# Kernel optimization log

Measured on AMD Instinct MI355X. Metric: run time of the kernel, lower is better.

## Reference

```python
import jax, jax.numpy as jnp
import numpy as np

# irreps_in = irreps_out = 32x0e + 16x1o ; irreps_sh = 1x0e + 1x1o
MUL0, MUL1 = 32, 16
N_NODES = 12000
N_EDGES = 120000
INV_SQRT3 = float(1.0 / np.sqrt(3.0))   # w3j(1,1,0), w3j(0,1,1), w3j(1,0,1) coefficient
SQRT2 = float(np.sqrt(2.0))             # e3nn normalize2mom constant for ReLU
# e3nn TP norms: irrep_normalization='component', path_normalization='element'.
# Each output irrep receives paths with num_elements 32 and 16 -> x = 48.
N_0E = float(1.0 / np.sqrt(48.0))       # alpha = dim(0e)/48 = 1/48
N_1O = float(np.sqrt(3.0 / 48.0))       # alpha = dim(1o)/48 = 3/48
# uvw weight blocks (mul2 = 1): (s,y0->s),(s,y0->g),(v,y1->s),(v,y1->g),(s,y1->v),(v,y0->v)
SPLITS = [MUL0 * MUL0, MUL0 * MUL1, MUL1 * MUL0, MUL1 * MUL1, MUL0 * MUL1, MUL1 * MUL1]
OFFS = np.cumsum([0] + SPLITS)
WNUM = int(OFFS[-1])  # 3072


def setup_inputs() -> dict:
    key = jax.random.key(0)
    k1, k2, k3, k4, k5 = jax.random.split(key, 5)
    x = jax.random.normal(k1, (N_NODES, MUL0 + 3 * MUL1), dtype=jnp.float32)
    edge_attr = jax.random.normal(k2, (N_EDGES, 64), dtype=jnp.float32)
    Yij = jax.random.normal(k3, (N_EDGES, 4), dtype=jnp.float32)
    edge_index = jax.random.randint(k4, (2, N_EDGES), 0, N_NODES, dtype=jnp.int64)
    w_emb = jax.random.normal(k5, (2 * MUL0 + 64, WNUM), dtype=jnp.float32)
    return {"x": x, "edge_attr": edge_attr, "Yij": Yij,
            "edge_index": edge_index, "w_emb": w_emb}


def reference(x, edge_attr, Yij, edge_index, w_emb):
    dst, src = edge_index[0], edge_index[1]
    E = edge_attr.shape[0]
    xs = x[:, :MUL0]                                   # [N, 32] scalars (0e)
    xv = x[:, MUL0:].reshape(-1, MUL1, 3)              # [N, 16, 3] vectors (1o)

    # per-edge weight MLP (single e3nn FC layer, weight scaled by 1/sqrt(fan_in))
    emb = jnp.concatenate([xs[dst], xs[src], edge_attr], axis=-1)     # [E, 128]
    w = emb @ (w_emb / np.sqrt(w_emb.shape[0]))                       # [E, 3072]
    Ws = [w[:, OFFS[i]:OFFS[i + 1]] for i in range(6)]
    W1 = Ws[0].reshape(E, MUL0, MUL0)
    W2 = Ws[1].reshape(E, MUL0, MUL1)
    W3 = Ws[2].reshape(E, MUL1, MUL0)
    W4 = Ws[3].reshape(E, MUL1, MUL1)
    W5 = Ws[4].reshape(E, MUL0, MUL1)
    W6 = Ws[5].reshape(E, MUL1, MUL1)

    # gather source features, split sh
    x1s, x1v = xs[src], xv[src]                        # [E,32], [E,16,3]
    y0, y1 = Yij[:, 0], Yij[:, 1:4]                    # [E], [E,3]

    sy0 = x1s * y0[:, None]                            # 0e x 0e paths
    vdot = jnp.einsum('euk,ek->eu', x1v, y1) * INV_SQRT3  # 1o x 1o -> 0e
    out_s = N_0E * (jnp.einsum('euw,eu->ew', W1, sy0) +
                    jnp.einsum('euw,eu->ew', W3, vdot))    # [E, 32]
    out_g = N_0E * (jnp.einsum('euw,eu->ew', W2, sy0) +
                    jnp.einsum('euw,eu->ew', W4, vdot))    # [E, 16]
    out_v = (N_1O * INV_SQRT3) * (
        jnp.einsum('euw,eu,ek->ewk', W5, x1s, y1) +
        jnp.einsum('euw,euk->ewk', W6, x1v * y0[:, None, None]))  # [E, 16, 3]

    msg = jnp.concatenate([out_s, out_g, out_v.reshape(E, MUL1 * 3)], axis=-1)  # [E, 96]

    # scatter mean onto destination nodes
    summed = jax.ops.segment_sum(msg, dst, num_segments=N_NODES)
    cnt = jax.ops.segment_sum(jnp.ones((E,), msg.dtype), dst, num_segments=N_NODES)
    mean = summed / jnp.maximum(cnt, 1.0)[:, None]

    # Gate (e3nn Activation normalizes ReLU by sqrt(2))
    s = SQRT2 * jax.nn.relu(mean[:, :MUL0])
    g = SQRT2 * jax.nn.relu(mean[:, MUL0:MUL0 + MUL1])
    v = mean[:, MUL0 + MUL1:].reshape(-1, MUL1, 3) * g[:, :, None]
    out = jnp.concatenate([s, v.reshape(-1, MUL1 * 3)], axis=-1)     # [N, 80]
    return x + out
```

## Files before the change

kernel.cpp:

```cpp
#include <hip/hip_runtime.h>
#include <hip/hip_bf16.h>

#define E_EDGES 120000
#define NUM_NODES 12000

typedef __attribute__((ext_vector_type(8))) short bfrag;
typedef __attribute__((ext_vector_type(8))) unsigned short ushort8;
typedef __attribute__((ext_vector_type(4))) float f32x4;

#define INV_SQRT3 0.57735026918962576f
#define SQRT2_C   1.41421356237309515f
#define N_0E_C    0.14433756729740643f
#define NV_C      0.14433756729740643f
#define WSCALE    0.08838834764831845f

__device__ __forceinline__ unsigned short f2bf(float f) {
    union { float f; unsigned int u; } v; v.f = f;
    unsigned int r = v.u + 0x7fffu + ((v.u >> 16) & 1u);
    return (unsigned short)(r >> 16);
}

__device__ __forceinline__ ushort8 pack8(f32x4 a, f32x4 b) {
    ushort8 o;
    o[0] = f2bf(a.x); o[1] = f2bf(a.y); o[2] = f2bf(a.z); o[3] = f2bf(a.w);
    o[4] = f2bf(b.x); o[5] = f2bf(b.y); o[6] = f2bf(b.z); o[7] = f2bf(b.w);
    return o;
}

__global__ void k_wt(const float* __restrict__ w_emb, unsigned short* __restrict__ Bt) {
    int o = blockIdx.x * 256 + threadIdx.x;
    if (o >= 3072 * 128) return;
    int t = o >> 11;
    int c = (o >> 3) & 255;
    int j = o & 7;
    int kb = c >> 6;
    int quad = (c >> 4) & 3;
    int col = c & 15;
    int k = kb * 32 + quad * 8 + j;
    int n = t * 16 + col;
    Bt[o] = f2bf(w_emb[k * 3072 + n] * WSCALE);
}

__global__ void k_prep(const float* __restrict__ x, const float* __restrict__ edge_attr,
                       const float* __restrict__ Yij, const int* __restrict__ edge_index,
                       unsigned short* __restrict__ emb, float* __restrict__ rT,
                       float* __restrict__ cnt) {
    int e = blockIdx.x * 256 + threadIdx.x;
    if (e >= E_EDGES) return;
    int dst = edge_index[e];
    int src = edge_index[E_EDGES + e];
    f32x4 y = *(const f32x4*)(Yij + 4 * (long)e);
    float y0 = y.x, y1a = y.y, y1b = y.z, y1c = y.w;
    const float* xd = x + (long)dst * 80;
    const float* xs = x + (long)src * 80;
    const float* ea = edge_attr + (long)e * 64;

    ushort8* embp = (ushort8*)(emb + (long)e * 128);

    float xsv[80];
#pragma unroll
    for (int i = 0; i < 80; i += 4) {
        f32x4 v = *(const f32x4*)(xs + i);
        xsv[i] = v.x; xsv[i + 1] = v.y; xsv[i + 2] = v.z; xsv[i + 3] = v.w;
    }
#pragma unroll
    for (int cb = 0; cb < 4; ++cb) {
        f32x4 a = *(const f32x4*)(xd + cb * 8);
        f32x4 b = *(const f32x4*)(xd + cb * 8 + 4);
        embp[cb] = pack8(a, b);
    }
#pragma unroll
    for (int cb = 0; cb < 4; ++cb) {
        f32x4 a, b;
        a.x = xsv[cb * 8 + 0]; a.y = xsv[cb * 8 + 1]; a.z = xsv[cb * 8 + 2]; a.w = xsv[cb * 8 + 3];
        b.x = xsv[cb * 8 + 4]; b.y = xsv[cb * 8 + 5]; b.z = xsv[cb * 8 + 6]; b.w = xsv[cb * 8 + 7];
        embp[4 + cb] = pack8(a, b);
    }
#pragma unroll
    for (int cb = 0; cb < 8; ++cb) {
        f32x4 a = *(const f32x4*)(ea + cb * 8);
        f32x4 b = *(const f32x4*)(ea + cb * 8 + 4);
        embp[8 + cb] = pack8(a, b);
    }
#pragma unroll
    for (int u = 0; u < 32; ++u) rT[(long)u * E_EDGES + e] = xsv[u] * y0;
#pragma unroll
    for (int u = 0; u < 16; ++u)
        rT[(long)(32 + u) * E_EDGES + e] =
            (xsv[32 + 3 * u] * y1a + xsv[33 + 3 * u] * y1b + xsv[34 + 3 * u] * y1c) * INV_SQRT3;
#pragma unroll
    for (int u = 0; u < 32; ++u) rT[(long)(48 + u) * E_EDGES + e] = xsv[u];
#pragma unroll
    for (int j = 0; j < 48; ++j) rT[(long)(80 + j) * E_EDGES + e] = xsv[32 + j] * y0;
    atomicAdd(cnt + dst, 1.0f);
}

__global__ __launch_bounds__(256, 4) void k_gemm(
    const unsigned short* __restrict__ emb, const unsigned short* __restrict__ Bt,
    const float* __restrict__ rT, const int* __restrict__ edge_index,
    const float* __restrict__ Yij, float* __restrict__ summed) {
    const int lane = threadIdx.x & 63;
    const int wave = threadIdx.x >> 6;
    const int phase = blockIdx.x & 1;
    long e0 = (long)(blockIdx.x >> 1) * 128 + (long)wave * 32;
    const bool dup = (e0 + 32 > E_EDGES);
    if (dup) e0 = E_EDGES - 32;
    const int col = lane & 15, quad = lane >> 4;

    __shared__ __align__(16) char lds[2][16384];

    bfrag A[2][4];
#pragma unroll
    for (int s = 0; s < 2; ++s) {
        const unsigned short* ap = emb + (e0 + s * 16 + col) * 128 + quad * 8;
#pragma unroll
        for (int kb = 0; kb < 4; ++kb) A[s][kb] = *(const bfrag*)(ap + kb * 32);
    }

    auto stage = [&](int ci) {
        const char* g = (const char*)Bt + (size_t)ci * 16384 + wave * 4096 + lane * 16;
        char* l = &lds[ci & 1][wave * 4096];
#pragma unroll
        for (int j = 0; j < 4; ++j)
            __builtin_amdgcn_global_load_lds(
                (const __attribute__((address_space(1))) unsigned int*)(g + j * 1024),
                (__attribute__((address_space(3))) unsigned int*)(l + j * 1024), 16, 0, 0);
    };

    f32x4 z = {0.f, 0.f, 0.f, 0.f};

    const float* rbase = rT + e0 + quad * 4;
    auto loadw = [&](int r, f32x4& a, f32x4& b) {
        const float* p = rbase + (long)r * E_EDGES;
        a = *(const f32x4*)(p);
        b = *(const f32x4*)(p + 16);
    };

    auto tile = [&](const char* lt, f32x4& c0, f32x4& c1) {
        bfrag B0 = *(const bfrag*)(lt + lane * 16);
        bfrag B1 = *(const bfrag*)(lt + lane * 16 + 1024);
        bfrag B2 = *(const bfrag*)(lt + lane * 16 + 2048);
        bfrag B3 = *(const bfrag*)(lt + lane * 16 + 3072);
        c0 = z; c1 = z;
        c0 = __builtin_amdgcn_mfma_f32_16x16x32_bf16(A[0][0], B0, c0, 0, 0, 0);
        c1 = __builtin_amdgcn_mfma_f32_16x16x32_bf16(A[1][0], B0, c1, 0, 0, 0);
        c0 = __builtin_amdgcn_mfma_f32_16x16x32_bf16(A[0][1], B1, c0, 0, 0, 0);
        c1 = __builtin_amdgcn_mfma_f32_16x16x32_bf16(A[1][1], B1, c1, 0, 0, 0);
        c0 = __builtin_amdgcn_mfma_f32_16x16x32_bf16(A[0][2], B2, c0, 0, 0, 0);
        c1 = __builtin_amdgcn_mfma_f32_16x16x32_bf16(A[1][2], B2, c1, 0, 0, 0);
        c0 = __builtin_amdgcn_mfma_f32_16x16x32_bf16(A[0][3], B3, c0, 0, 0, 0);
        c1 = __builtin_amdgcn_mfma_f32_16x16x32_bf16(A[1][3], B3, c1, 0, 0, 0);
    };

    int bufp = 0;
    auto nextbuf = [&](int nxt) -> const char* {
        __syncthreads();
        if (nxt >= 0) stage(nxt);
        const char* b = lds[bufp & 1];
        ++bufp;
        return b;
    };

    f32x4 c0, c1;

    if (phase == 0) {
        f32x4 acc_s0[2] = {z, z}, acc_s1[2] = {z, z};
        stage(0);
        {
            f32x4 p0a, p0b, p1a, p1b;
            loadw(0, p0a, p0b); loadw(1, p1a, p1b);
#pragma unroll 1
            for (int j = 0; j < 16; ++j) {
                const char* buf = nextbuf(j < 15 ? j + 1 : 24);
                f32x4 w0a = p0a, w0b = p0b, w1a = p1a, w1b = p1b;
                int nr = (j < 15) ? (2 * j + 2) : 32;
                loadw(nr, p0a, p0b); loadw(nr + 1, p1a, p1b);
                tile(buf,         c0, c1); acc_s0[0] += c0 * w0a; acc_s0[1] += c1 * w0b;
                tile(buf + 4096,  c0, c1); acc_s1[0] += c0 * w0a; acc_s1[1] += c1 * w0b;
                tile(buf + 8192,  c0, c1); acc_s0[0] += c0 * w1a; acc_s0[1] += c1 * w1b;
                tile(buf + 12288, c0, c1); acc_s1[0] += c0 * w1a; acc_s1[1] += c1 * w1b;
            }
        }
        {
            f32x4 p0a, p0b, p1a, p1b;
            loadw(32, p0a, p0b); loadw(33, p1a, p1b);
#pragma unroll 1
            for (int j = 0; j < 8; ++j) {
                const char* buf = nextbuf(j < 7 ? 25 + j : -1);
                f32x4 w0a = p0a, w0b = p0b, w1a = p1a, w1b = p1b;
                int nr = (j < 7) ? (32 + 2 * j + 2) : 32;
                loadw(nr, p0a, p0b); loadw(nr + 1, p1a, p1b);
                tile(buf,         c0, c1); acc_s0[0] += c0 * w0a; acc_s0[1] += c1 * w0b;
                tile(buf + 4096,  c0, c1); acc_s1[0] += c0 * w0a; acc_s1[1] += c1 * w0b;
                tile(buf + 8192,  c0, c1); acc_s0[0] += c0 * w1a; acc_s0[1] += c1 * w1b;
                tile(buf + 12288, c0, c1); acc_s1[0] += c0 * w1a; acc_s1[1] += c1 * w1b;
            }
        }
        if (dup) return;
#pragma unroll
        for (int s = 0; s < 2; ++s) {
            long eb = e0 + s * 16 + quad * 4;
#pragma unroll
            for (int r = 0; r < 4; ++r) {
                int d = edge_index[eb + r];
                float* base = summed + (long)d * 96;
                atomicAdd(base + col,      N_0E_C * acc_s0[s][r]);
                atomicAdd(base + col + 16, N_0E_C * acc_s1[s][r]);
            }
        }
    } else {
        f32x4 acc_g[2] = {z, z}, acc_t5[2] = {z, z};
        f32x4 acc_v[2][3] = {{z, z, z}, {z, z, z}};
        stage(16);
        {
            f32x4 pa[4], pb[4];
#pragma unroll
            for (int i = 0; i < 4; ++i) loadw(i, pa[i], pb[i]);
#pragma unroll 1
            for (int j = 0; j < 8; ++j) {
                const char* buf = nextbuf(j < 7 ? 17 + j : 32);
                f32x4 wa[4], wb[4];
#pragma unroll
                for (int i = 0; i < 4; ++i) { wa[i] = pa[i]; wb[i] = pb[i]; }
                int nr = (j < 7) ? (4 * j + 4) : 32;
#pragma unroll
                for (int i = 0; i < 4; ++i) loadw(nr + i, pa[i], pb[i]);
#pragma unroll
                for (int i = 0; i < 4; ++i) {
                    tile(buf + i * 4096, c0, c1);
                    acc_g[0] += c0 * wa[i]; acc_g[1] += c1 * wb[i];
                }
            }
        }
        {
            f32x4 pa[4], pb[4];
#pragma unroll
            for (int i = 0; i < 4; ++i) loadw(32 + i, pa[i], pb[i]);
#pragma unroll 1
            for (int j = 0; j < 4; ++j) {
                const char* buf = nextbuf(33 + j);
                f32x4 wa[4], wb[4];
#pragma unroll
                for (int i = 0; i < 4; ++i) { wa[i] = pa[i]; wb[i] = pb[i]; }
                int nr = (j < 3) ? (32 + 4 * j + 4) : 48;
#pragma unroll
                for (int i = 0; i < 4; ++i) loadw(nr + i, pa[i], pb[i]);
#pragma unroll
                for (int i = 0; i < 4; ++i) {
                    tile(buf + i * 4096, c0, c1);
                    acc_g[0] += c0 * wa[i]; acc_g[1] += c1 * wb[i];
                }
            }
        }
        {
            f32x4 pa[4], pb[4];
#pragma unroll
            for (int i = 0; i < 4; ++i) loadw(48 + i, pa[i], pb[i]);
#pragma unroll 1
            for (int j = 0; j < 8; ++j) {
                const char* buf = nextbuf(37 + j);
                f32x4 wa[4], wb[4];
#pragma unroll
                for (int i = 0; i < 4; ++i) { wa[i] = pa[i]; wb[i] = pb[i]; }
                int nr = (j < 7) ? (48 + 4 * j + 4) : 48;
#pragma unroll
                for (int i = 0; i < 4; ++i) loadw(nr + i, pa[i], pb[i]);
#pragma unroll
                for (int i = 0; i < 4; ++i) {
                    tile(buf + i * 4096, c0, c1);
                    acc_t5[0] += c0 * wa[i]; acc_t5[1] += c1 * wb[i];
                }
            }
        }
        {
            f32x4 va[3], vb[3];
#pragma unroll
            for (int k = 0; k < 3; ++k) loadw(80 + k, va[k], vb[k]);
#pragma unroll 1
            for (int j = 0; j < 4; ++j) {
                const char* buf = nextbuf(j < 3 ? 45 + j : -1);
#pragma unroll
                for (int i = 0; i < 4; ++i) {
                    f32x4 wa[3], wb[3];
#pragma unroll
                    for (int k = 0; k < 3; ++k) { wa[k] = va[k]; wb[k] = vb[k]; }
                    int un = 4 * j + i + 1; if (un > 15) un = 0;
#pragma unroll
                    for (int k = 0; k < 3; ++k) loadw(80 + 3 * un + k, va[k], vb[k]);
                    tile(buf + i * 4096, c0, c1);
#pragma unroll
                    for (int k = 0; k < 3; ++k) {
                        acc_v[0][k] += c0 * wa[k];
                        acc_v[1][k] += c1 * wb[k];
                    }
                }
            }
        }
        if (dup) return;
#pragma unroll
        for (int s = 0; s < 2; ++s) {
            long eb = e0 + s * 16 + quad * 4;
#pragma unroll
            for (int r = 0; r < 4; ++r) {
                long e = eb + r;
                int d = edge_index[e];
                float* base = summed + (long)d * 96;
                float y1a = Yij[4 * e + 1], y1b = Yij[4 * e + 2], y1c = Yij[4 * e + 3];
                atomicAdd(base + 32 + col, N_0E_C * acc_g[s][r]);
                float t5 = acc_t5[s][r];
                atomicAdd(base + 48 + col * 3 + 0, NV_C * (t5 * y1a + acc_v[s][0][r]));
                atomicAdd(base + 48 + col * 3 + 1, NV_C * (t5 * y1b + acc_v[s][1][r]));
                atomicAdd(base + 48 + col * 3 + 2, NV_C * (t5 * y1c + acc_v[s][2][r]));
            }
        }
    }
}

__global__ void k_final(const float* __restrict__ x, const float* __restrict__ summed,
                        const float* __restrict__ cnt, float* __restrict__ out) {
    int tid = blockIdx.x * 256 + threadIdx.x;
    if (tid >= NUM_NODES * 80) return;
    int n = tid / 80, c = tid % 80;
    float m = fmaxf(cnt[n], 1.0f);
    float inv = 1.0f / m;
    float val;
    if (c < 32) {
        val = SQRT2_C * fmaxf(summed[(long)n * 96 + c] * inv, 0.0f);
    } else {
        int j = c - 32;
        int w = j / 3;
        float g = SQRT2_C * fmaxf(summed[(long)n * 96 + 32 + w] * inv, 0.0f);
        val = summed[(long)n * 96 + 48 + j] * inv * g;
    }
    out[tid] = x[tid] + val;
}

extern "C" void kernel_launch(void* const* d_in, const int* in_sizes, int n_in,
                              void* d_out, int out_size, void* d_ws, size_t ws_size,
                              hipStream_t stream) {
    const float* x         = (const float*)d_in[0];
    const float* edge_attr = (const float*)d_in[1];
    const float* Yij       = (const float*)d_in[2];
    const int*   edge_index= (const int*)d_in[3];
    const float* w_emb     = (const float*)d_in[4];
    float* out = (float*)d_out;

    char* ws = (char*)d_ws;
    size_t off = 0;
    unsigned short* emb = (unsigned short*)(ws + off); off += (size_t)E_EDGES * 128 * 2;
    unsigned short* Bt  = (unsigned short*)(ws + off); off += (size_t)3072 * 128 * 2;
    off = (off + 255) & ~(size_t)255;
    float* rT     = (float*)(ws + off); off += (size_t)128 * E_EDGES * 4;
    size_t zoff = off;
    float* summed = (float*)(ws + off); off += (size_t)NUM_NODES * 96 * 4;
    float* cnt    = (float*)(ws + off); off += (size_t)NUM_NODES * 4;

    hipMemsetAsync(ws + zoff, 0, (size_t)NUM_NODES * 97 * 4, stream);
    k_wt  <<<(3072 * 128 + 255) / 256, 256, 0, stream>>>(w_emb, Bt);
    k_prep<<<(E_EDGES + 255) / 256, 256, 0, stream>>>(x, edge_attr, Yij, edge_index, emb, rT, cnt);
    k_gemm<<<2 * ((E_EDGES + 127) / 128), 256, 0, stream>>>(emb, Bt, rT, edge_index, Yij, summed);
    k_final<<<(NUM_NODES * 80 + 255) / 256, 256, 0, stream>>>(x, summed, cnt, out);
}
```

Before: 293.8 us.

## Tile rT per 32-edge block, double LDS stage size, coalesce weight transpose

Stores the per-edge coefficient array rT as contiguous 32-edge by 128-row blocks instead of row-major over all edges, so each wave's coefficient loads hit a compact 16KB region. The GEMM now stages 32KB chunks of the weight matrix into LDS per barrier, which halves the number of __syncthreads, and launch bounds drop to 2 blocks per SM to fit the larger LDS. The weight transpose kernel now reads w_emb coalesced and scatters the writes. Possible costs are lower occupancy and fewer overlapping waves.

```diff
diff --git a/kernel.cpp b/kernel.cpp
--- a/kernel.cpp
+++ b/kernel.cpp
@@ -28,17 +28,13 @@
 }
 
 __global__ void k_wt(const float* __restrict__ w_emb, unsigned short* __restrict__ Bt) {
-    int o = blockIdx.x * 256 + threadIdx.x;
-    if (o >= 3072 * 128) return;
-    int t = o >> 11;
-    int c = (o >> 3) & 255;
-    int j = o & 7;
-    int kb = c >> 6;
-    int quad = (c >> 4) & 3;
-    int col = c & 15;
-    int k = kb * 32 + quad * 8 + j;
-    int n = t * 16 + col;
-    Bt[o] = f2bf(w_emb[k * 3072 + n] * WSCALE);
+    int i = blockIdx.x * 256 + threadIdx.x;
+    if (i >= 128 * 3072) return;
+    int k = i / 3072;
+    int n = i - k * 3072;
+    int t = n >> 4, col = n & 15;
+    int kb = k >> 5, quad = (k >> 3) & 3, j = k & 7;
+    Bt[(size_t)t * 2048 + (size_t)(kb * 64 + quad * 16 + col) * 8 + j] = f2bf(w_emb[i] * WSCALE);
 }
 
 __global__ void k_prep(const float* __restrict__ x, const float* __restrict__ edge_attr,
@@ -56,6 +52,7 @@
     const float* ea = edge_attr + (long)e * 64;
 
     ushort8* embp = (ushort8*)(emb + (long)e * 128);
+    float* rb = rT + (long)(e >> 5) * 4096 + (e & 31);
 
     float xsv[80];
 #pragma unroll
@@ -83,19 +80,19 @@
         embp[8 + cb] = pack8(a, b);
     }
 #pragma unroll
-    for (int u = 0; u < 32; ++u) rT[(long)u * E_EDGES + e] = xsv[u] * y0;
+    for (int u = 0; u < 32; ++u) rb[u * 32] = xsv[u] * y0;
 #pragma unroll
     for (int u = 0; u < 16; ++u)
-        rT[(long)(32 + u) * E_EDGES + e] =
+        rb[(32 + u) * 32] =
             (xsv[32 + 3 * u] * y1a + xsv[33 + 3 * u] * y1b + xsv[34 + 3 * u] * y1c) * INV_SQRT3;
 #pragma unroll
-    for (int u = 0; u < 32; ++u) rT[(long)(48 + u) * E_EDGES + e] = xsv[u];
-#pragma unroll
-    for (int j = 0; j < 48; ++j) rT[(long)(80 + j) * E_EDGES + e] = xsv[32 + j] * y0;
+    for (int u = 0; u < 32; ++u) rb[(48 + u) * 32] = xsv[u];
+#pragma unroll
+    for (int j = 0; j < 48; ++j) rb[(80 + j) * 32] = xsv[32 + j] * y0;
     atomicAdd(cnt + dst, 1.0f);
 }
 
-__global__ __launch_bounds__(256, 4) void k_gemm(
+__global__ __launch_bounds__(256, 2) void k_gemm(
     const unsigned short* __restrict__ emb, const unsigned short* __restrict__ Bt,
     const float* __restrict__ rT, const int* __restrict__ edge_index,
     const float* __restrict__ Yij, float* __restrict__ summed) {
@@ -107,7 +104,7 @@
     if (dup) e0 = E_EDGES - 32;
     const int col = lane & 15, quad = lane >> 4;
 
-    __shared__ __align__(16) char lds[2][16384];
+    __shared__ __align__(16) char lds[2][32768];
 
     bfrag A[2][4];
 #pragma unroll
@@ -117,21 +114,26 @@
         for (int kb = 0; kb < 4; ++kb) A[s][kb] = *(const bfrag*)(ap + kb * 32);
     }
 
+    int wp = 0, rp = 0;
     auto stage = [&](int ci) {
-        const char* g = (const char*)Bt + (size_t)ci * 16384 + wave * 4096 + lane * 16;
-        char* l = &lds[ci & 1][wave * 4096];
-#pragma unroll
-        for (int j = 0; j < 4; ++j)
+        const char* g = (const char*)Bt + (size_t)ci * 32768 + wave * 8192 + lane * 16;
+        char* l = &lds[(wp++) & 1][wave * 8192];
+#pragma unroll
+        for (int j = 0; j < 8; ++j)
             __builtin_amdgcn_global_load_lds(
                 (const __attribute__((address_space(1))) unsigned int*)(g + j * 1024),
                 (__attribute__((address_space(3))) unsigned int*)(l + j * 1024), 16, 0, 0);
     };
+    auto nextbuf = [&](int nxt) -> const char* {
+        __syncthreads();
+        if (nxt >= 0) stage(nxt);
+        return lds[(rp++) & 1];
+    };
 
     f32x4 z = {0.f, 0.f, 0.f, 0.f};
-
-    const float* rbase = rT + e0 + quad * 4;
+    const float* rbase = rT + ((e0 >> 5) * 4096) + quad * 4;
     auto loadw = [&](int r, f32x4& a, f32x4& b) {
-        const float* p = rbase + (long)r * E_EDGES;
+        const float* p = rbase + r * 32;
         a = *(const f32x4*)(p);
         b = *(const f32x4*)(p + 16);
     };
@@ -152,49 +154,51 @@
         c1 = __builtin_amdgcn_mfma_f32_16x16x32_bf16(A[1][3], B3, c1, 0, 0, 0);
     };
 
-    int bufp = 0;
-    auto nextbuf = [&](int nxt) -> const char* {
-        __syncthreads();
-        if (nxt >= 0) stage(nxt);
-        const char* b = lds[bufp & 1];
-        ++bufp;
-        return b;
-    };
-
     f32x4 c0, c1;
 
     if (phase == 0) {
         f32x4 acc_s0[2] = {z, z}, acc_s1[2] = {z, z};
+        f32x4 ca[4], cb[4], na[4], nb[4];
         stage(0);
-        {
-            f32x4 p0a, p0b, p1a, p1b;
-            loadw(0, p0a, p0b); loadw(1, p1a, p1b);
-#pragma unroll 1
-            for (int j = 0; j < 16; ++j) {
-                const char* buf = nextbuf(j < 15 ? j + 1 : 24);
-                f32x4 w0a = p0a, w0b = p0b, w1a = p1a, w1b = p1b;
-                int nr = (j < 15) ? (2 * j + 2) : 32;
-                loadw(nr, p0a, p0b); loadw(nr + 1, p1a, p1b);
-                tile(buf,         c0, c1); acc_s0[0] += c0 * w0a; acc_s0[1] += c1 * w0b;
-                tile(buf + 4096,  c0, c1); acc_s1[0] += c0 * w0a; acc_s1[1] += c1 * w0b;
-                tile(buf + 8192,  c0, c1); acc_s0[0] += c0 * w1a; acc_s0[1] += c1 * w1b;
-                tile(buf + 12288, c0, c1); acc_s1[0] += c0 * w1a; acc_s1[1] += c1 * w1b;
-            }
-        }
-        {
-            f32x4 p0a, p0b, p1a, p1b;
-            loadw(32, p0a, p0b); loadw(33, p1a, p1b);
-#pragma unroll 1
-            for (int j = 0; j < 8; ++j) {
-                const char* buf = nextbuf(j < 7 ? 25 + j : -1);
-                f32x4 w0a = p0a, w0b = p0b, w1a = p1a, w1b = p1b;
-                int nr = (j < 7) ? (32 + 2 * j + 2) : 32;
-                loadw(nr, p0a, p0b); loadw(nr + 1, p1a, p1b);
-                tile(buf,         c0, c1); acc_s0[0] += c0 * w0a; acc_s0[1] += c1 * w0b;
-                tile(buf + 4096,  c0, c1); acc_s1[0] += c0 * w0a; acc_s1[1] += c1 * w0b;
-                tile(buf + 8192,  c0, c1); acc_s0[0] += c0 * w1a; acc_s0[1] += c1 * w1b;
-                tile(buf + 12288, c0, c1); acc_s1[0] += c0 * w1a; acc_s1[1] += c1 * w1b;
-            }
+#pragma unroll
+        for (int i = 0; i < 4; ++i) loadw(i, ca[i], cb[i]);
+#pragma unroll 1
+        for (int bc = 0; bc < 8; ++bc) {
+            const char* buf = nextbuf(bc < 7 ? bc + 1 : 12);
+            int nr = (bc < 7) ? 4 * bc + 4 : 32;
+#pragma unroll
+            for (int i = 0; i < 4; ++i) loadw(nr + i, na[i], nb[i]);
+#pragma unroll
+            for (int h = 0; h < 2; ++h) {
+                const char* hb = buf + h * 16384;
+                f32x4 w0a = ca[2 * h], w0b = cb[2 * h];
+                f32x4 w1a = ca[2 * h + 1], w1b = cb[2 * h + 1];
+                tile(hb,         c0, c1); acc_s0[0] += c0 * w0a; acc_s0[1] += c1 * w0b;
+                tile(hb + 4096,  c0, c1); acc_s1[0] += c0 * w0a; acc_s1[1] += c1 * w0b;
+                tile(hb + 8192,  c0, c1); acc_s0[0] += c0 * w1a; acc_s0[1] += c1 * w1b;
+                tile(hb + 12288, c0, c1); acc_s1[0] += c0 * w1a; acc_s1[1] += c1 * w1b;
+            }
+#pragma unroll
+            for (int i = 0; i < 4; ++i) { ca[i] = na[i]; cb[i] = nb[i]; }
+        }
+#pragma unroll 1
+        for (int bc = 0; bc < 4; ++bc) {
+            const char* buf = nextbuf(bc < 3 ? 13 + bc : -1);
+            int nr = (bc < 3) ? 36 + 4 * bc : 32;
+#pragma unroll
+            for (int i = 0; i < 4; ++i) loadw(nr + i, na[i], nb[i]);
+#pragma unroll
+            for (int h = 0; h < 2; ++h) {
+                const char* hb = buf + h * 16384;
+                f32x4 w0a = ca[2 * h], w0b = cb[2 * h];
+                f32x4 w1a = ca[2 * h + 1], w1b = cb[2 * h + 1];
+                tile(hb,         c0, c1); acc_s0[0] += c0 * w0a; acc_s0[1] += c1 * w0b;
+                tile(hb + 4096,  c0, c1); acc_s1[0] += c0 * w0a; acc_s1[1] += c1 * w0b;
+                tile(hb + 8192,  c0, c1); acc_s0[0] += c0 * w1a; acc_s0[1] += c1 * w1b;
+                tile(hb + 12288, c0, c1); acc_s1[0] += c0 * w1a; acc_s1[1] += c1 * w1b;
+            }
+#pragma unroll
+            for (int i = 0; i < 4; ++i) { ca[i] = na[i]; cb[i] = nb[i]; }
         }
         if (dup) return;
 #pragma unroll
@@ -211,14 +215,16 @@
     } else {
         f32x4 acc_g[2] = {z, z}, acc_t5[2] = {z, z};
         f32x4 acc_v[2][3] = {{z, z, z}, {z, z, z}};
-        stage(16);
+        stage(8);
+        const char* buf = nullptr;
         {
             f32x4 pa[4], pb[4];
 #pragma unroll
             for (int i = 0; i < 4; ++i) loadw(i, pa[i], pb[i]);
 #pragma unroll 1
             for (int j = 0; j < 8; ++j) {
-                const char* buf = nextbuf(j < 7 ? 17 + j : 32);
+                if ((j & 1) == 0) { int bc = j >> 1; buf = nextbuf(bc < 3 ? 9 + bc : 16); }
+                else buf += 16384;
                 f32x4 wa[4], wb[4];
 #pragma unroll
                 for (int i = 0; i < 4; ++i) { wa[i] = pa[i]; wb[i] = pb[i]; }
@@ -238,11 +244,12 @@
             for (int i = 0; i < 4; ++i) loadw(32 + i, pa[i], pb[i]);
 #pragma unroll 1
             for (int j = 0; j < 4; ++j) {
-                const char* buf = nextbuf(33 + j);
+                if ((j & 1) == 0) buf = nextbuf(j == 0 ? 17 : 18);
+                else buf += 16384;
                 f32x4 wa[4], wb[4];
 #pragma unroll
                 for (int i = 0; i < 4; ++i) { wa[i] = pa[i]; wb[i] = pb[i]; }
-                int nr = (j < 3) ? (32 + 4 * j + 4) : 48;
+                int nr = (j < 3) ? (36 + 4 * j) : 48;
 #pragma unroll
                 for (int i = 0; i < 4; ++i) loadw(nr + i, pa[i], pb[i]);
 #pragma unroll
@@ -258,11 +265,12 @@
             for (int i = 0; i < 4; ++i) loadw(48 + i, pa[i], pb[i]);
 #pragma unroll 1
             for (int j = 0; j < 8; ++j) {
-                const char* buf = nextbuf(37 + j);
+                if ((j & 1) == 0) { int bc = j >> 1; buf = nextbuf(bc < 3 ? 19 + bc : 22); }
+                else buf += 16384;
                 f32x4 wa[4], wb[4];
 #pragma unroll
                 for (int i = 0; i < 4; ++i) { wa[i] = pa[i]; wb[i] = pb[i]; }
-                int nr = (j < 7) ? (48 + 4 * j + 4) : 48;
+                int nr = (j < 7) ? (52 + 4 * j) : 48;
 #pragma unroll
                 for (int i = 0; i < 4; ++i) loadw(nr + i, pa[i], pb[i]);
 #pragma unroll
@@ -278,7 +286,8 @@
             for (int k = 0; k < 3; ++k) loadw(80 + k, va[k], vb[k]);
 #pragma unroll 1
             for (int j = 0; j < 4; ++j) {
-                const char* buf = nextbuf(j < 3 ? 45 + j : -1);
+                if ((j & 1) == 0) buf = nextbuf(j == 0 ? 23 : -1);
+                else buf += 16384;
 #pragma unroll
                 for (int i = 0; i < 4; ++i) {
                     f32x4 wa[3], wb[3];
@@ -350,13 +359,13 @@
     unsigned short* emb = (unsigned short*)(ws + off); off += (size_t)E_EDGES * 128 * 2;
     unsigned short* Bt  = (unsigned short*)(ws + off); off += (size_t)3072 * 128 * 2;
     off = (off + 255) & ~(size_t)255;
-    float* rT     = (float*)(ws + off); off += (size_t)128 * E_EDGES * 4;
+    float* rT     = (float*)(ws + off); off += (size_t)(E_EDGES / 32) * 4096 * 4;
     size_t zoff = off;
     float* summed = (float*)(ws + off); off += (size_t)NUM_NODES * 96 * 4;
     float* cnt    = (float*)(ws + off); off += (size_t)NUM_NODES * 4;
 
     hipMemsetAsync(ws + zoff, 0, (size_t)NUM_NODES * 97 * 4, stream);
-    k_wt  <<<(3072 * 128 + 255) / 256, 256, 0, stream>>>(w_emb, Bt);
+    k_wt  <<<(128 * 3072 + 255) / 256, 256, 0, stream>>>(w_emb, Bt);
     k_prep<<<(E_EDGES + 255) / 256, 256, 0, stream>>>(x, edge_attr, Yij, edge_index, emb, rT, cnt);
     k_gemm<<<2 * ((E_EDGES + 127) / 128), 256, 0, stream>>>(emb, Bt, rT, edge_index, Yij, summed);
     k_final<<<(NUM_NODES * 80 + 255) / 256, 256, 0, stream>>>(x, summed, cnt, out);
```

New measurement: 295.3 us. About the same (+0.5%).

## Replace atomic scatter with CSR gather and merge GEMM phases per block

Applied to the files above, without the earlier changes.

Float atomics into the summed buffer are replaced by writing per-edge messages to a buffer. A new histogram, scan and fill stage builds a CSR edge list per destination node, and k_final gathers each node's messages and reduces them. The GEMM kernel no longer splits work across two block phases; each block computes all outputs for its edges, so the emb A fragments are loaded once. The rT buffer is re-tiled into 32-edge chunks, and k_wt reads w_emb coalesced. The cost is extra message traffic (E×96 floats), added launches including a single-block scan, and uncoalesced per-edge gathers in the final kernel.

```diff
diff --git a/kernel.cpp b/kernel.cpp
--- a/kernel.cpp
+++ b/kernel.cpp
@@ -28,23 +28,19 @@
 }
 
 __global__ void k_wt(const float* __restrict__ w_emb, unsigned short* __restrict__ Bt) {
-    int o = blockIdx.x * 256 + threadIdx.x;
-    if (o >= 3072 * 128) return;
-    int t = o >> 11;
-    int c = (o >> 3) & 255;
-    int j = o & 7;
-    int kb = c >> 6;
-    int quad = (c >> 4) & 3;
-    int col = c & 15;
-    int k = kb * 32 + quad * 8 + j;
-    int n = t * 16 + col;
-    Bt[o] = f2bf(w_emb[k * 3072 + n] * WSCALE);
+    int i = blockIdx.x * 256 + threadIdx.x;
+    if (i >= 128 * 3072) return;
+    int k = i / 3072;
+    int n = i - k * 3072;
+    int t = n >> 4, col = n & 15;
+    int kb = k >> 5, quad = (k >> 3) & 3, j = k & 7;
+    Bt[(size_t)t * 2048 + (size_t)(kb * 64 + quad * 16 + col) * 8 + j] = f2bf(w_emb[i] * WSCALE);
 }
 
 __global__ void k_prep(const float* __restrict__ x, const float* __restrict__ edge_attr,
                        const float* __restrict__ Yij, const int* __restrict__ edge_index,
                        unsigned short* __restrict__ emb, float* __restrict__ rT,
-                       float* __restrict__ cnt) {
+                       int* __restrict__ hist) {
     int e = blockIdx.x * 256 + threadIdx.x;
     if (e >= E_EDGES) return;
     int dst = edge_index[e];
@@ -56,6 +52,7 @@
     const float* ea = edge_attr + (long)e * 64;
 
     ushort8* embp = (ushort8*)(emb + (long)e * 128);
+    float* rb = rT + (size_t)(e >> 5) * 4096 + (e & 31);
 
     float xsv[80];
 #pragma unroll
@@ -83,26 +80,63 @@
         embp[8 + cb] = pack8(a, b);
     }
 #pragma unroll
-    for (int u = 0; u < 32; ++u) rT[(long)u * E_EDGES + e] = xsv[u] * y0;
+    for (int u = 0; u < 32; ++u) rb[u * 32] = xsv[u] * y0;
 #pragma unroll
     for (int u = 0; u < 16; ++u)
-        rT[(long)(32 + u) * E_EDGES + e] =
+        rb[(32 + u) * 32] =
             (xsv[32 + 3 * u] * y1a + xsv[33 + 3 * u] * y1b + xsv[34 + 3 * u] * y1c) * INV_SQRT3;
 #pragma unroll
-    for (int u = 0; u < 32; ++u) rT[(long)(48 + u) * E_EDGES + e] = xsv[u];
-#pragma unroll
-    for (int j = 0; j < 48; ++j) rT[(long)(80 + j) * E_EDGES + e] = xsv[32 + j] * y0;
-    atomicAdd(cnt + dst, 1.0f);
+    for (int u = 0; u < 32; ++u) rb[(48 + u) * 32] = xsv[u];
+#pragma unroll
+    for (int j = 0; j < 48; ++j) rb[(80 + j) * 32] = xsv[32 + j] * y0;
+    atomicAdd(hist + dst, 1);
+}
+
+__global__ __launch_bounds__(1024) void k_scan(const int* __restrict__ hist,
+                                               int* __restrict__ off, int* __restrict__ pos) {
+    __shared__ int part[1024];
+    int t = threadIdx.x;
+    int base = t * 12;
+    int loc[12];
+    int s = 0;
+#pragma unroll
+    for (int i = 0; i < 12; ++i) {
+        int idx = base + i;
+        int v = (idx < NUM_NODES) ? hist[idx] : 0;
+        loc[i] = s; s += v;
+    }
+    part[t] = s;
+    __syncthreads();
+    for (int ofs = 1; ofs < 1024; ofs <<= 1) {
+        int v = (t >= ofs) ? part[t - ofs] : 0;
+        __syncthreads();
+        part[t] += v;
+        __syncthreads();
+    }
+    int pre = (t == 0) ? 0 : part[t - 1];
+#pragma unroll
+    for (int i = 0; i < 12; ++i) {
+        int idx = base + i;
+        if (idx < NUM_NODES) { off[idx] = pre + loc[i]; pos[idx] = pre + loc[i]; }
+    }
+}
+
+__global__ void k_fill(const int* __restrict__ edge_index, int* __restrict__ pos,
+                       int* __restrict__ csr_e) {
+    int e = blockIdx.x * 256 + threadIdx.x;
+    if (e >= E_EDGES) return;
+    int d = edge_index[e];
+    int p = atomicAdd(pos + d, 1);
+    csr_e[p] = e;
 }
 
 __global__ __launch_bounds__(256, 4) void k_gemm(
     const unsigned short* __restrict__ emb, const unsigned short* __restrict__ Bt,
-    const float* __restrict__ rT, const int* __restrict__ edge_index,
-    const float* __restrict__ Yij, float* __restrict__ summed) {
+    const float* __restrict__ rT, const float* __restrict__ Yij,
+    float* __restrict__ msg) {
     const int lane = threadIdx.x & 63;
     const int wave = threadIdx.x >> 6;
-    const int phase = blockIdx.x & 1;
-    long e0 = (long)(blockIdx.x >> 1) * 128 + (long)wave * 32;
+    long e0 = (long)blockIdx.x * 128 + (long)wave * 32;
     const bool dup = (e0 + 32 > E_EDGES);
     if (dup) e0 = E_EDGES - 32;
     const int col = lane & 15, quad = lane >> 4;
@@ -117,21 +151,29 @@
         for (int kb = 0; kb < 4; ++kb) A[s][kb] = *(const bfrag*)(ap + kb * 32);
     }
 
+    int wp = 0, rp = 0;
     auto stage = [&](int ci) {
         const char* g = (const char*)Bt + (size_t)ci * 16384 + wave * 4096 + lane * 16;
-        char* l = &lds[ci & 1][wave * 4096];
+        char* l = &lds[(wp++) & 1][wave * 4096];
 #pragma unroll
         for (int j = 0; j < 4; ++j)
             __builtin_amdgcn_global_load_lds(
                 (const __attribute__((address_space(1))) unsigned int*)(g + j * 1024),
                 (__attribute__((address_space(3))) unsigned int*)(l + j * 1024), 16, 0, 0);
     };
+    auto nextbuf = [&](int nxt) -> const char* {
+        __syncthreads();
+        if (nxt >= 0) stage(nxt);
+        return lds[(rp++) & 1];
+    };
 
     f32x4 z = {0.f, 0.f, 0.f, 0.f};
-
-    const float* rbase = rT + e0 + quad * 4;
+    f32x4 acc_s0[2] = {z, z}, acc_s1[2] = {z, z}, acc_g[2] = {z, z}, acc_t5[2] = {z, z};
+    f32x4 acc_v[2][3] = {{z, z, z}, {z, z, z}};
+
+    const float* rbase = rT + (size_t)(e0 >> 5) * 4096 + quad * 4;
     auto loadw = [&](int r, f32x4& a, f32x4& b) {
-        const float* p = rbase + (long)r * E_EDGES;
+        const float* p = rbase + r * 32;
         a = *(const f32x4*)(p);
         b = *(const f32x4*)(p + 16);
     };
@@ -152,187 +194,174 @@
         c1 = __builtin_amdgcn_mfma_f32_16x16x32_bf16(A[1][3], B3, c1, 0, 0, 0);
     };
 
-    int bufp = 0;
-    auto nextbuf = [&](int nxt) -> const char* {
-        __syncthreads();
-        if (nxt >= 0) stage(nxt);
-        const char* b = lds[bufp & 1];
-        ++bufp;
-        return b;
-    };
-
     f32x4 c0, c1;
 
-    if (phase == 0) {
-        f32x4 acc_s0[2] = {z, z}, acc_s1[2] = {z, z};
+    {
+        f32x4 p0a, p0b, p1a, p1b;
         stage(0);
-        {
-            f32x4 p0a, p0b, p1a, p1b;
-            loadw(0, p0a, p0b); loadw(1, p1a, p1b);
-#pragma unroll 1
-            for (int j = 0; j < 16; ++j) {
-                const char* buf = nextbuf(j < 15 ? j + 1 : 24);
-                f32x4 w0a = p0a, w0b = p0b, w1a = p1a, w1b = p1b;
-                int nr = (j < 15) ? (2 * j + 2) : 32;
-                loadw(nr, p0a, p0b); loadw(nr + 1, p1a, p1b);
-                tile(buf,         c0, c1); acc_s0[0] += c0 * w0a; acc_s0[1] += c1 * w0b;
-                tile(buf + 4096,  c0, c1); acc_s1[0] += c0 * w0a; acc_s1[1] += c1 * w0b;
-                tile(buf + 8192,  c0, c1); acc_s0[0] += c0 * w1a; acc_s0[1] += c1 * w1b;
-                tile(buf + 12288, c0, c1); acc_s1[0] += c0 * w1a; acc_s1[1] += c1 * w1b;
+        loadw(0, p0a, p0b); loadw(1, p1a, p1b);
+#pragma unroll 1
+        for (int j = 0; j < 16; ++j) {
+            const char* buf = nextbuf(j < 15 ? j + 1 : 16);
+            f32x4 w0a = p0a, w0b = p0b, w1a = p1a, w1b = p1b;
+            int nr = (j < 15) ? (2 * j + 2) : 0;
+            loadw(nr, p0a, p0b); loadw(nr + 1, p1a, p1b);
+            tile(buf,         c0, c1); acc_s0[0] += c0 * w0a; acc_s0[1] += c1 * w0b;
+            tile(buf + 4096,  c0, c1); acc_s1[0] += c0 * w0a; acc_s1[1] += c1 * w0b;
+            tile(buf + 8192,  c0, c1); acc_s0[0] += c0 * w1a; acc_s0[1] += c1 * w1b;
+            tile(buf + 12288, c0, c1); acc_s1[0] += c0 * w1a; acc_s1[1] += c1 * w1b;
+        }
+    }
+    {
+        f32x4 pa[4], pb[4];
+#pragma unroll
+        for (int i = 0; i < 4; ++i) loadw(i, pa[i], pb[i]);
+#pragma unroll 1
+        for (int j = 0; j < 8; ++j) {
+            const char* buf = nextbuf(j < 7 ? 17 + j : 24);
+            f32x4 wa[4], wb[4];
+#pragma unroll
+            for (int i = 0; i < 4; ++i) { wa[i] = pa[i]; wb[i] = pb[i]; }
+            int nr = (j < 7) ? (4 * j + 4) : 32;
+#pragma unroll
+            for (int i = 0; i < 4; ++i) loadw(nr + i, pa[i], pb[i]);
+#pragma unroll
+            for (int i = 0; i < 4; ++i) {
+                tile(buf + i * 4096, c0, c1);
+                acc_g[0] += c0 * wa[i]; acc_g[1] += c1 * wb[i];
             }
         }
-        {
-            f32x4 p0a, p0b, p1a, p1b;
-            loadw(32, p0a, p0b); loadw(33, p1a, p1b);
-#pragma unroll 1
-            for (int j = 0; j < 8; ++j) {
-                const char* buf = nextbuf(j < 7 ? 25 + j : -1);
-                f32x4 w0a = p0a, w0b = p0b, w1a = p1a, w1b = p1b;
-                int nr = (j < 7) ? (32 + 2 * j + 2) : 32;
-                loadw(nr, p0a, p0b); loadw(nr + 1, p1a, p1b);
-                tile(buf,         c0, c1); acc_s0[0] += c0 * w0a; acc_s0[1] += c1 * w0b;
-                tile(buf + 4096,  c0, c1); acc_s1[0] += c0 * w0a; acc_s1[1] += c1 * w0b;
-                tile(buf + 8192,  c0, c1); acc_s0[0] += c0 * w1a; acc_s0[1] += c1 * w1b;
-                tile(buf + 12288, c0, c1); acc_s1[0] += c0 * w1a; acc_s1[1] += c1 * w1b;
+    }
+    {
+        f32x4 p0a, p0b, p1a, p1b;
+        loadw(32, p0a, p0b); loadw(33, p1a, p1b);
+#pragma unroll 1
+        for (int j = 0; j < 8; ++j) {
+            const char* buf = nextbuf(j < 7 ? 25 + j : 32);
+            f32x4 w0a = p0a, w0b = p0b, w1a = p1a, w1b = p1b;
+            int nr = (j < 7) ? (32 + 2 * j + 2) : 32;
+            loadw(nr, p0a, p0b); loadw(nr + 1, p1a, p1b);
+            tile(buf,         c0, c1); acc_s0[0] += c0 * w0a; acc_s0[1] += c1 * w0b;
+            tile(buf + 4096,  c0, c1); acc_s1[0] += c0 * w0a; acc_s1[1] += c1 * w0b;
+            tile(buf + 8192,  c0, c1); acc_s0[0] += c0 * w1a; acc_s0[1] += c1 * w1b;
+            tile(buf + 12288, c0, c1); acc_s1[0] += c0 * w1a; acc_s1[1] += c1 * w1b;
+        }
+    }
+    {
+        f32x4 pa[4], pb[4];
+#pragma unroll
+        for (int i = 0; i < 4; ++i) loadw(32 + i, pa[i], pb[i]);
+#pragma unroll 1
+        for (int j = 0; j < 4; ++j) {
+            const char* buf = nextbuf(33 + j);
+            f32x4 wa[4], wb[4];
+#pragma unroll
+            for (int i = 0; i < 4; ++i) { wa[i] = pa[i]; wb[i] = pb[i]; }
+            int nr = (j < 3) ? (32 + 4 * j + 4) : 48;
+#pragma unroll
+            for (int i = 0; i < 4; ++i) loadw(nr + i, pa[i], pb[i]);
+#pragma unroll
+            for (int i = 0; i < 4; ++i) {
+                tile(buf + i * 4096, c0, c1);
+                acc_g[0] += c0 * wa[i]; acc_g[1] += c1 * wb[i];
             }
         }
-        if (dup) return;
-#pragma unroll
-        for (int s = 0; s < 2; ++s) {
-            long eb = e0 + s * 16 + quad * 4;
-#pragma unroll
-            for (int r = 0; r < 4; ++r) {
-                int d = edge_index[eb + r];
-                float* base = summed + (long)d * 96;
-                atomicAdd(base + col,      N_0E_C * acc_s0[s][r]);
-                atomicAdd(base + col + 16, N_0E_C * acc_s1[s][r]);
+    }
+    {
+        f32x4 pa[4], pb[4];
+#pragma unroll
+        for (int i = 0; i < 4; ++i) loadw(48 + i, pa[i], pb[i]);
+#pragma unroll 1
+        for (int j = 0; j < 8; ++j) {
+            const char* buf = nextbuf(37 + j);
+            f32x4 wa[4], wb[4];
+#pragma unroll
+            for (int i = 0; i < 4; ++i) { wa[i] = pa[i]; wb[i] = pb[i]; }
+            int nr = (j < 7) ? (48 + 4 * j + 4) : 48;
+#pragma unroll
+            for (int i = 0; i < 4; ++i) loadw(nr + i, pa[i], pb[i]);
+#pragma unroll
+            for (int i = 0; i < 4; ++i) {
+                tile(buf + i * 4096, c0, c1);
+                acc_t5[0] += c0 * wa[i]; acc_t5[1] += c1 * wb[i];
             }
         }
-    } else {
-        f32x4 acc_g[2] = {z, z}, acc_t5[2] = {z, z};
-        f32x4 acc_v[2][3] = {{z, z, z}, {z, z, z}};
-        stage(16);
-        {
-            f32x4 pa[4], pb[4];
-#pragma unroll
-            for (int i = 0; i < 4; ++i) loadw(i, pa[i], pb[i]);
-#pragma unroll 1
-            for (int j = 0; j < 8; ++j) {
-                const char* buf = nextbuf(j < 7 ? 17 + j : 32);
-                f32x4 wa[4], wb[4];
-#pragma unroll
-                for (int i = 0; i < 4; ++i) { wa[i] = pa[i]; wb[i] = pb[i]; }
-                int nr = (j < 7) ? (4 * j + 4) : 32;
-#pragma unroll
-                for (int i = 0; i < 4; ++i) loadw(nr + i, pa[i], pb[i]);
-#pragma unroll
-                for (int i = 0; i < 4; ++i) {
-                    tile(buf + i * 4096, c0, c1);
-                    acc_g[0] += c0 * wa[i]; acc_g[1] += c1 * wb[i];
+    }
+    {
+        f32x4 va[3], vb[3];
+#pragma unroll
+        for (int k = 0; k < 3; ++k) loadw(80 + k, va[k], vb[k]);
+#pragma unroll 1
+        for (int j = 0; j < 4; ++j) {
+            const char* buf = nextbuf(j < 3 ? 45 + j : -1);
+#pragma unroll
+            for (int i = 0; i < 4; ++i) {
+                f32x4 wa[3], wb[3];
+#pragma unroll
+                for (int k = 0; k < 3; ++k) { wa[k] = va[k]; wb[k] = vb[k]; }
+                int un = 4 * j + i + 1; if (un > 15) un = 0;
+#pragma unroll
+                for (int k = 0; k < 3; ++k) loadw(80 + 3 * un + k, va[k], vb[k]);
+                tile(buf + i * 4096, c0, c1);
+#pragma unroll
+                for (int k = 0; k < 3; ++k) {
+                    acc_v[0][k] += c0 * wa[k];
+                    acc_v[1][k] += c1 * wb[k];
                 }
             }
         }
-        {
-            f32x4 pa[4], pb[4];
-#pragma unroll
-            for (int i = 0; i < 4; ++i) loadw(32 + i, pa[i], pb[i]);
-#pragma unroll 1
-            for (int j = 0; j < 4; ++j) {
-                const char* buf = nextbuf(33 + j);
-                f32x4 wa[4], wb[4];
-#pragma unroll
-                for (int i = 0; i < 4; ++i) { wa[i] = pa[i]; wb[i] = pb[i]; }
-                int nr = (j < 3) ? (32 + 4 * j + 4) : 48;
-#pragma unroll
-                for (int i = 0; i < 4; ++i) loadw(nr + i, pa[i], pb[i]);
-#pragma unroll
-                for (int i = 0; i < 4; ++i) {
-                    tile(buf + i * 4096, c0, c1);
-                    acc_g[0] += c0 * wa[i]; acc_g[1] += c1 * wb[i];
-                }
-            }
-        }
-        {
-            f32x4 pa[4], pb[4];
-#pragma unroll
-            for (int i = 0; i < 4; ++i) loadw(48 + i, pa[i], pb[i]);
-#pragma unroll 1
-            for (int j = 0; j < 8; ++j) {
-                const char* buf = nextbuf(37 + j);
-                f32x4 wa[4], wb[4];
-#pragma unroll
-                for (int i = 0; i < 4; ++i) { wa[i] = pa[i]; wb[i] = pb[i]; }
-                int nr = (j < 7) ? (48 + 4 * j + 4) : 48;
-#pragma unroll
-                for (int i = 0; i < 4; ++i) loadw(nr + i, pa[i], pb[i]);
-#pragma unroll
-                for (int i = 0; i < 4; ++i) {
-                    tile(buf + i * 4096, c0, c1);
-                    acc_t5[0] += c0 * wa[i]; acc_t5[1] += c1 * wb[i];
-                }
-            }
-        }
-        {
-            f32x4 va[3], vb[3];
-#pragma unroll
-            for (int k = 0; k < 3; ++k) loadw(80 + k, va[k], vb[k]);
-#pragma unroll 1
-            for (int j = 0; j < 4; ++j) {
-                const char* buf = nextbuf(j < 3 ? 45 + j : -1);
-#pragma unroll
-                for (int i = 0; i < 4; ++i) {
-                    f32x4 wa[3], wb[3];
-#pragma unroll
-                    for (int k = 0; k < 3; ++k) { wa[k] = va[k]; wb[k] = vb[k]; }
-                    int un = 4 * j + i + 1; if (un > 15) un = 0;
-#pragma unroll
-                    for (int k = 0; k < 3; ++k) loadw(80 + 3 * un + k, va[k], vb[k]);
-                    tile(buf + i * 4096, c0, c1);
-#pragma unroll
-                    for (int k = 0; k < 3; ++k) {
-                        acc_v[0][k] += c0 * wa[k];
-                        acc_v[1][k] += c1 * wb[k];
-                    }
-                }
-            }
-        }
-        if (dup) return;
-#pragma unroll
-        for (int s = 0; s < 2; ++s) {
-            long eb = e0 + s * 16 + quad * 4;
-#pragma unroll
-            for (int r = 0; r < 4; ++r) {
-                long e = eb + r;
-                int d = edge_index[e];
-                float* base = summed + (long)d * 96;
-                float y1a = Yij[4 * e + 1], y1b = Yij[4 * e + 2], y1c = Yij[4 * e + 3];
-                atomicAdd(base + 32 + col, N_0E_C * acc_g[s][r]);
-                float t5 = acc_t5[s][r];
-                atomicAdd(base + 48 + col * 3 + 0, NV_C * (t5 * y1a + acc_v[s][0][r]));
-                atomicAdd(base + 48 + col * 3 + 1, NV_C * (t5 * y1b + acc_v[s][1][r]));
-                atomicAdd(base + 48 + col * 3 + 2, NV_C * (t5 * y1c + acc_v[s][2][r]));
-            }
-        }
-    }
-}
-
-__global__ void k_final(const float* __restrict__ x, const float* __restrict__ summed,
-                        const float* __restrict__ cnt, float* __restrict__ out) {
-    int tid = blockIdx.x * 256 + threadIdx.x;
-    if (tid >= NUM_NODES * 80) return;
-    int n = tid / 80, c = tid % 80;
-    float m = fmaxf(cnt[n], 1.0f);
-    float inv = 1.0f / m;
-    float val;
-    if (c < 32) {
-        val = SQRT2_C * fmaxf(summed[(long)n * 96 + c] * inv, 0.0f);
-    } else {
-        int j = c - 32;
-        int w = j / 3;
-        float g = SQRT2_C * fmaxf(summed[(long)n * 96 + 32 + w] * inv, 0.0f);
-        val = summed[(long)n * 96 + 48 + j] * inv * g;
-    }
-    out[tid] = x[tid] + val;
+    }
+
+    if (dup) return;
+#pragma unroll
+    for (int s = 0; s < 2; ++s) {
+        long eb = e0 + s * 16 + quad * 4;
+#pragma unroll
+        for (int r = 0; r < 4; ++r) {
+            long e = eb + r;
+            float* m = msg + (size_t)e * 96;
+            float y1a = Yij[4 * e + 1], y1b = Yij[4 * e + 2], y1c = Yij[4 * e + 3];
+            m[col]      = N_0E_C * acc_s0[s][r];
+            m[16 + col] = N_0E_C * acc_s1[s][r];
+            m[32 + col] = N_0E_C * acc_g[s][r];
+            float t5 = acc_t5[s][r];
+            m[48 + col] = NV_C * (t5 * y1a + acc_v[s][0][r]);
+            m[64 + col] = NV_C * (t5 * y1b + acc_v[s][1][r]);
+            m[80 + col] = NV_C * (t5 * y1c + acc_v[s][2][r]);
+        }
+    }
+}
+
+__global__ __launch_bounds__(128) void k_final(
+    const float* __restrict__ x, const float* __restrict__ msg,
+    const int* __restrict__ hist, const int* __restrict__ off,
+    const int* __restrict__ csr_e, float* __restrict__ out) {
+    int n = blockIdx.x;
+    int t = threadIdx.x;
+    __shared__ float sm[96];
+    int cnt = hist[n];
+    int o = off[n];
+    if (t < 96) {
+        float s = 0.f;
+        for (int j = 0; j < cnt; ++j) {
+            int e = csr_e[o + j];
+            s += msg[(size_t)e * 96 + t];
+        }
+        float m = (cnt > 0) ? (float)cnt : 1.0f;
+        sm[t] = s / m;
+    }
+    __syncthreads();
+    if (t < 80) {
+        float val;
+        if (t < 32) {
+            val = SQRT2_C * fmaxf(sm[t], 0.f);
+        } else {
+            int j = t - 32, w = j / 3, k = j - 3 * w;
+            float g = SQRT2_C * fmaxf(sm[32 + w], 0.f);
+            val = sm[48 + k * 16 + w] * g;
+        }
+        out[(size_t)n * 80 + t] = x[(size_t)n * 80 + t] + val;
+    }
 }
 
 extern "C" void kernel_launch(void* const* d_in, const int* in_sizes, int n_in,
@@ -346,18 +375,22 @@
     float* out = (float*)d_out;
 
     char* ws = (char*)d_ws;
-    size_t off = 0;
-    unsigned short* emb = (unsigned short*)(ws + off); off += (size_t)E_EDGES * 128 * 2;
-    unsigned short* Bt  = (unsigned short*)(ws + off); off += (size_t)3072 * 128 * 2;
-    off = (off + 255) & ~(size_t)255;
-    float* rT     = (float*)(ws + off); off += (size_t)128 * E_EDGES * 4;
-    size_t zoff = off;
-    float* summed = (float*)(ws + off); off += (size_t)NUM_NODES * 96 * 4;
-    float* cnt    = (float*)(ws + off); off += (size_t)NUM_NODES * 4;
-
-    hipMemsetAsync(ws + zoff, 0, (size_t)NUM_NODES * 97 * 4, stream);
-    k_wt  <<<(3072 * 128 + 255) / 256, 256, 0, stream>>>(w_emb, Bt);
-    k_prep<<<(E_EDGES + 255) / 256, 256, 0, stream>>>(x, edge_attr, Yij, edge_index, emb, rT, cnt);
-    k_gemm<<<2 * ((E_EDGES + 127) / 128), 256, 0, stream>>>(emb, Bt, rT, edge_index, Yij, summed);
-    k_final<<<(NUM_NODES * 80 + 255) / 256, 256, 0, stream>>>(x, summed, cnt, out);
-}
+    size_t off_b = 0;
+    unsigned short* emb = (unsigned short*)(ws + off_b); off_b += (size_t)E_EDGES * 128 * 2;
+    unsigned short* Bt  = (unsigned short*)(ws + off_b); off_b += (size_t)3072 * 128 * 2;
+    off_b = (off_b + 255) & ~(size_t)255;
+    float* rT   = (float*)(ws + off_b); off_b += (size_t)(E_EDGES / 32) * 4096 * 4;
+    float* msg  = (float*)(ws + off_b); off_b += (size_t)E_EDGES * 96 * 4;
+    int* hist   = (int*)(ws + off_b);   off_b += (size_t)NUM_NODES * 4;
+    int* offv   = (int*)(ws + off_b);   off_b += (size_t)NUM_NODES * 4;
+    int* pos    = (int*)(ws + off_b);   off_b += (size_t)NUM_NODES * 4;
+    int* csr_e  = (int*)(ws + off_b);   off_b += (size_t)E_EDGES * 4;
+
+    hipMemsetAsync(hist, 0, (size_t)NUM_NODES * 4, stream);
+    k_wt  <<<(128 * 3072 + 255) / 256, 256, 0, stream>>>(w_emb, Bt);
+    k_prep<<<(E_EDGES + 255) / 256, 256, 0, stream>>>(x, edge_attr, Yij, edge_index, emb, rT, hist);
+    k_scan<<<1, 1024, 0, stream>>>(hist, offv, pos);
+    k_fill<<<(E_EDGES + 255) / 256, 256, 0, stream>>>(edge_index, pos, csr_e);
+    k_gemm<<<(E_EDGES + 127) / 128, 256, 0, stream>>>(emb, Bt, rT, Yij, msg);
+    k_final<<<NUM_NODES, 128, 0, stream>>>(x, msg, hist, offv, csr_e, out);
+}
```

After: 308.2 us. +4.9%, slower.
